# Kernel tuning notes

Hardware: AMD Instinct MI355X
Metric: run time of the kernel (lower is better)

The kernel has to match this reference:

```python
import jax, jax.numpy as jnp
import numpy as np

N_NODES = 50000
N_EDGES = 800000
D = 128  # in_dim == hidden_dim
N_CLASSES = 2


def setup_inputs() -> dict:
    key = jax.random.key(0)
    ks = jax.random.split(key, 8)
    x = jax.random.normal(ks[0], (N_NODES, D), dtype=jnp.float32)
    edge_index = jax.random.randint(ks[1], (2, N_EDGES), 0, N_NODES)
    s = 1.0 / np.sqrt(D)
    W1 = jax.random.normal(ks[2], (D, D), dtype=jnp.float32) * s
    b1 = jnp.zeros((D,), jnp.float32)
    W2 = jax.random.normal(ks[3], (D, D), dtype=jnp.float32) * s
    b2 = jnp.zeros((D,), jnp.float32)
    Wc = jax.random.normal(ks[4], (D, N_CLASSES), dtype=jnp.float32) * s
    bc = jnp.zeros((N_CLASSES,), jnp.float32)
    return {"x": x, "edge_index": edge_index, "W1": W1, "b1": b1,
            "W2": W2, "b2": b2, "Wc": Wc, "bc": bc}


def gcn_layer(x, W, b, src, dst, n):
    """PyG GCNConv: h = D^{-1/2}(A+I)D^{-1/2} (x @ W) + b, self-loops added."""
    h = x @ W  # [n, d_out]
    loop = jnp.arange(n)
    src2 = jnp.concatenate([src, loop])  # [E+n]
    dst2 = jnp.concatenate([dst, loop])
    deg = jax.ops.segment_sum(jnp.ones_like(dst2, dtype=h.dtype), dst2, num_segments=n)
    inv_sqrt = jax.lax.rsqrt(deg)  # deg >= 1 thanks to self-loops
    coef = inv_sqrt[src2] * inv_sqrt[dst2]  # [E+n]
    msg = h[src2] * coef[:, None]  # gather + scale
    out = jax.ops.segment_sum(msg, dst2, num_segments=n)  # scatter-add
    return out + b


def reference(x, edge_index, W1, b1, W2, b2, Wc, bc):
    src, dst = edge_index[0], edge_index[1]
    n = x.shape[0]
    h = jax.nn.relu(gcn_layer(x, W1, b1, src, dst, n))
    h = jax.nn.relu(gcn_layer(h, W2, b2, src, dst, n))
    g = h.mean(axis=0)  # mean pool over nodes -> [hidden]
    logits = g @ Wc + bc  # [2]
    return jax.nn.log_softmax(logits, axis=0)
```

## Files before the change

kernel.cpp:

```cpp
#include <hip/hip_runtime.h>

#define D 128
#define PAD 64
#define SCAP 12288
typedef unsigned char  u8;
typedef unsigned short u16;
typedef unsigned int   u32;
typedef unsigned long long u64;
typedef __attribute__((ext_vector_type(8))) short bf16x8;
typedef __attribute__((ext_vector_type(4))) float f32x4;
typedef __attribute__((ext_vector_type(2))) float f32x2;


__device__ __forceinline__ float b2f_lo(u32 w) {
    u32 x = w << 16; float f; __builtin_memcpy(&f, &x, 4); return f;
}
__device__ __forceinline__ float b2f_hi(u32 w) {
    u32 x = w & 0xffff0000u; float f; __builtin_memcpy(&f, &x, 4); return f;
}
__device__ __forceinline__ u16 f2b(float f) {
    u32 x; __builtin_memcpy(&x, &f, 4);
    u32 lsb = (x >> 16) & 1u;
    x += 0x7fffu + lsb;
    return (u16)(x >> 16);
}
__device__ __forceinline__ u8 f2fp8(float f) {
    int p = __builtin_amdgcn_cvt_pk_fp8_f32(f, f, 0, false);
    return (u8)(p & 0xff);
}
__device__ __forceinline__ f32x2 fp8lo(u32 w) {
    return __builtin_amdgcn_cvt_pk_f32_fp8((int)w, false);
}
__device__ __forceinline__ f32x2 fp8hi(u32 w) {
    return __builtin_amdgcn_cvt_pk_f32_fp8((int)w, true);
}

__global__ void k_init(float* __restrict__ gpool,
                       const void* p0, const void* p1, const void* p2, const void* p3,
                       const void* p4, const void* p5, const void* p6,
                       int* __restrict__ flags, u16* __restrict__ WTf1,
                       u16* __restrict__ WTf2,
                       const int* __restrict__ src, const int* __restrict__ dst, int E,
                       u32* __restrict__ slist, int* __restrict__ slcur, int pb) {
    __shared__ __align__(16) u16 t[128 * 130];
    __shared__ int s_wbf;
    __shared__ u32 lcnt[128], lbase[128], boff[128];
    const int bid = blockIdx.x, tid = threadIdx.x;
    if (bid == 0) {
        uint4* g4 = (uint4*)gpool;
        #pragma unroll
        for (int k = 0; k < 8; ++k) g4[tid + k * 256] = (uint4){0, 0, 0, 0};
        const void* ps[7] = {p0, p1, p2, p3, p4, p5, p6};
        const int   nw[7] = {64, 64, 64, 64, 64, 64, 1};
        int wave = tid >> 6, lane = tid & 63;
        for (int b = wave; b < 7; b += 4) {
            u32 w = (lane < nw[b]) ? ((const u32*)ps[b])[lane] : 0u;
            int nzb = (w != 0u);
            u32 e = (w >> 7) & 0xFFu;
            int hitb = nzb && (e > 100u && e < 140u);
            u64 nzm = __ballot(nzb);
            u64 hm  = __ballot(hitb);
            int nz = __popcll(nzm), hits = __popcll(hm);
            if (lane == 0) flags[b] = (nz == 0) || (2 * hits >= nz);
        }
        return;
    }
    if (bid >= 3) {
        const int pid = bid - 3;
        const int E4 = E >> 2;
        u32* stg = (u32*)t;
        if (tid < 128) lcnt[tid] = 0;
        __syncthreads();
        u32 wpk[8]; int gg[8]; u32 loc[8]; int vld[2];
        #pragma unroll
        for (int h = 0; h < 2; ++h) {
            const int i4 = pid * 512 + h * 256 + tid;
            vld[h] = i4 < E4;
            if (vld[h]) {
                int4 dd = ((const int4*)dst)[i4];
                int4 sv = ((const int4*)src)[i4];
                int d[4] = {dd.x, dd.y, dd.z, dd.w};
                int s[4] = {sv.x, sv.y, sv.z, sv.w};
                #pragma unroll
                for (int k = 0; k < 4; ++k) {
                    int e = h * 4 + k;
                    gg[e]  = d[k] >> 9;
                    wpk[e] = ((u32)d[k] << 16) | (u32)(s[k] & 0xffff);
                    loc[e] = atomicAdd(&lcnt[gg[e]], 1u);
                }
            }
        }
        __syncthreads();
        if (tid < 128) boff[tid] = lcnt[tid];
        __syncthreads();
        for (int o = 1; o < 128; o <<= 1) {
            u32 v = 0;
            if (tid < 128 && tid >= o) v = boff[tid - o];
            __syncthreads();
            if (tid < 128) boff[tid] += v;
            __syncthreads();
        }
        if (tid < 128) {
            u32 c = lcnt[tid];
            lbase[tid] = c ? atomicAdd((u32*)&slcur[tid], c) : 0u;
            boff[tid] -= c;
        }
        __syncthreads();
        #pragma unroll
        for (int h = 0; h < 2; ++h) {
            if (vld[h]) {
                #pragma unroll
                for (int k = 0; k < 4; ++k) {
                    int e = h * 4 + k;
                    stg[boff[gg[e]] + loc[e]] = wpk[e];
                }
            }
        }
        __syncthreads();
        const int tot = (int)(boff[127] + lcnt[127]);
        for (int j = tid; j < tot; j += 256) {
            u32 w = stg[j];
            int g = (int)(w >> 25);
            u32 p = lbase[g] + (u32)j - boff[g];
            if (p < SCAP) slist[(size_t)g * SCAP + p] = w;
        }
        if (pid == pb - 1 && tid < (E & 3)) {
            int e = (E & ~3) + tid;
            int d = dst[e], s = src[e];
            u32 p = atomicAdd((u32*)&slcur[d >> 9], 1u);
            if (p < SCAP) slist[(size_t)(d >> 9) * SCAP + p] = ((u32)d << 16) | (u32)(s & 0xffff);
        }
        return;
    }
    const void* Wp = (bid == 1) ? p1 : p3;
    u16* WTf      = (bid == 1) ? WTf1 : WTf2;
    if (tid < 64) {
        u32 w = ((const u32*)Wp)[tid];
        int nzb = (w != 0u);
        u32 e = (w >> 7) & 0xFFu;
        int hitb = nzb && (e > 100u && e < 140u);
        u64 nzm = __ballot(nzb);
        u64 hm  = __ballot(hitb);
        if (tid == 0) {
            int nz = __popcll(nzm), hits = __popcll(hm);
            s_wbf = (nz == 0) || (2 * hits >= nz);
        }
    }
    __syncthreads();
    if (s_wbf) {
        const u32* W2w = (const u32*)Wp;
        for (int i = tid; i < 8192; i += 256) {
            u32 w = W2w[i];
            int k = i >> 6, n2 = (i & 63) * 2;
            t[k * 130 + n2]     = (u16)(w & 0xffffu);
            t[k * 130 + n2 + 1] = (u16)(w >> 16);
        }
    } else {
        const float* Wf = (const float*)Wp;
        for (int i = tid; i < 16384; i += 256) {
            int k = i >> 7, nn = i & 127;
            t[k * 130 + nn] = f2b(Wf[i]);
        }
    }
    __syncthreads();
    for (int fi = tid; fi < 16384; fi += 256) {
        int j = fi & 7, lane = (fi >> 3) & 63, tc = fi >> 9;
        int tt = tc >> 3, c = tc & 7, m = lane & 15, quad = lane >> 4;
        int k = tt * 32 + quad * 8 + j, col = c * 16 + m;
        WTf[fi] = t[k * 130 + col];
    }
}

__global__ __launch_bounds__(256) void k_fused(
        const void* __restrict__ Ap, const u16* __restrict__ WTf1,
        const int* __restrict__ flags, u8* __restrict__ C, int n, int gb1, int fb0,
        int nsl, const u32* __restrict__ slist, const int* __restrict__ slcur,
        int* __restrict__ cnt, float* __restrict__ inv, u16* __restrict__ csrp) {
    __shared__ __align__(16) u8 sbuf[32768];
    __shared__ int lc[512];
    const int tid = threadIdx.x;
    if (blockIdx.x < (u32)gb1) {
        __shared__ int s_abf;
        u16* wfrag = (u16*)sbuf;
        for (int i = tid; i < 2048; i += 256)
            ((uint4*)wfrag)[i] = ((const uint4*)WTf1)[i];
        if (tid == 0) s_abf = flags[0];
        __syncthreads();
        const int abf = s_abf;
        const int wv = tid >> 6, lane = tid & 63;
        const int m = lane & 15, quad = lane >> 4;
        const int r0 = blockIdx.x * 128 + wv * 32;
        int ar0 = r0 + m;      if (ar0 > n - 1) ar0 = n - 1;
        int ar1 = r0 + 16 + m; if (ar1 > n - 1) ar1 = n - 1;

        bf16x8 a0[4], a1[4];
        if (abf) {
            const u16* A0 = (const u16*)Ap + (size_t)ar0 * D + quad * 8;
            const u16* A1 = (const u16*)Ap + (size_t)ar1 * D + quad * 8;
            #pragma unroll
            for (int t = 0; t < 4; ++t) {
                a0[t] = *(const bf16x8*)(A0 + t * 32);
                a1[t] = *(const bf16x8*)(A1 + t * 32);
            }
        } else {
            const float* A0 = (const float*)Ap + (size_t)ar0 * D + quad * 8;
            const float* A1 = (const float*)Ap + (size_t)ar1 * D + quad * 8;
            #pragma unroll
            for (int t = 0; t < 4; ++t) {
                float4 f0 = *(const float4*)(A0 + t * 32);
                float4 f1 = *(const float4*)(A0 + t * 32 + 4);
                float4 g0 = *(const float4*)(A1 + t * 32);
                float4 g1 = *(const float4*)(A1 + t * 32 + 4);
                bf16x8 a, b;
                a[0] = (short)f2b(f0.x); a[1] = (short)f2b(f0.y);
                a[2] = (short)f2b(f0.z); a[3] = (short)f2b(f0.w);
                a[4] = (short)f2b(f1.x); a[5] = (short)f2b(f1.y);
                a[6] = (short)f2b(f1.z); a[7] = (short)f2b(f1.w);
                b[0] = (short)f2b(g0.x); b[1] = (short)f2b(g0.y);
                b[2] = (short)f2b(g0.z); b[3] = (short)f2b(g0.w);
                b[4] = (short)f2b(g1.x); b[5] = (short)f2b(g1.y);
                b[6] = (short)f2b(g1.z); b[7] = (short)f2b(g1.w);
                a0[t] = a; a1[t] = b;
            }
        }
        f32x4 acc0[8], acc1[8];
        #pragma unroll
        for (int c = 0; c < 8; ++c) {
            acc0[c] = (f32x4){0.f, 0.f, 0.f, 0.f};
            acc1[c] = (f32x4){0.f, 0.f, 0.f, 0.f};
        }
        #pragma unroll
        for (int t = 0; t < 4; ++t) {
            #pragma unroll
            for (int c = 0; c < 8; ++c) {
                bf16x8 b = *(const bf16x8*)(wfrag + ((size_t)(t * 8 + c) * 64 + lane) * 8);
                acc0[c] = __builtin_amdgcn_mfma_f32_16x16x32_bf16(a0[t], b, acc0[c], 0, 0, 0);
                acc1[c] = __builtin_amdgcn_mfma_f32_16x16x32_bf16(a1[t], b, acc1[c], 0, 0, 0);
            }
        }
        __syncthreads();
        #pragma unroll
        for (int c = 0; c < 8; ++c) {
            #pragma unroll
            for (int r = 0; r < 4; ++r) {
                int lr = wv * 32 + quad * 4 + r;
                sbuf[lr * 132 + c * 16 + m]        = f2fp8(acc0[c][r]);
                sbuf[(lr + 16) * 132 + c * 16 + m] = f2fp8(acc1[c][r]);
            }
        }
        __syncthreads();
        int lr = tid >> 1, off = (tid & 1) * 64;
        int grow = blockIdx.x * 128 + lr;
        if (grow < n) {
            const u8* rp = sbuf + lr * 132 + off;
            uint4 v0 = *(const uint4*)(rp);
            uint4 v1 = *(const uint4*)(rp + 16);
            uint4 v2 = *(const uint4*)(rp + 32);
            uint4 v3 = *(const uint4*)(rp + 48);
            u8* gp = C + (size_t)grow * D + off;
            *(uint4*)(gp)      = v0;
            *(uint4*)(gp + 16) = v1;
            *(uint4*)(gp + 32) = v2;
            *(uint4*)(gp + 48) = v3;
        }
        return;
    }
    if (blockIdx.x < (u32)fb0) return;
    const int s = blockIdx.x - fb0;
    if (s >= nsl) return;
    const int base = s << 9;
    lc[tid] = 0; lc[tid + 256] = 0;
    __syncthreads();
    int len = slcur[s]; if (len > SCAP) len = SCAP;
    const u32* sl = slist + (size_t)s * SCAP;
    for (int e = tid; e < len; e += 256) {
        u32 w = sl[e];
        int d = (int)(w >> 16);
        int pos = atomicAdd(&lc[d - base], 1);
        if (pos < PAD) csrp[(size_t)d * PAD + pos] = (u16)(w & 0xffffu);
    }
    __syncthreads();
    #pragma unroll
    for (int i = tid; i < 512; i += 256) {
        int node = base + i;
        if (node < n) {
            int c = lc[i];
            cnt[node] = c;
            inv[node] = rsqrtf(1.0f + (float)c);
        }
    }
}

template<bool PRE>
__device__ __forceinline__ f32x4 agg_row4(int node, int lane, float invd, int mcnt,
                                          const u8* __restrict__ H,
                                          const u16* __restrict__ csrp,
                                          const float* __restrict__ inv,
                                          const void* __restrict__ bias, int bbf) {
    const int q = lane & 31, half = lane >> 5;
    int idx = csrp[(size_t)node * PAD + lane];
    f32x4 acc = (f32x4){0.f, 0.f, 0.f, 0.f};
    const int NP = (mcnt + 1) >> 1;
    int p = 0;
    for (; p + 8 <= NP; p += 8) {
        u32 w[8]; float sc[8]; int ok[8];
        #pragma unroll
        for (int k = 0; k < 8; ++k) {
            int e = 2 * (p + k) + half;
            int s = __shfl(idx, e);
            w[k] = *(const u32*)(H + (size_t)s * D + q * 4);
            if (!PRE) sc[k] = inv[s];
            ok[k] = e < mcnt;
        }
        #pragma unroll
        for (int k = 0; k < 8; ++k) {
            if (ok[k]) {
                f32x2 lo = fp8lo(w[k]), hi = fp8hi(w[k]);
                if (PRE) {
                    acc[0] += lo[0]; acc[1] += lo[1]; acc[2] += hi[0]; acc[3] += hi[1];
                } else {
                    acc[0] = fmaf(lo[0], sc[k], acc[0]);
                    acc[1] = fmaf(lo[1], sc[k], acc[1]);
                    acc[2] = fmaf(hi[0], sc[k], acc[2]);
                    acc[3] = fmaf(hi[1], sc[k], acc[3]);
                }
            }
        }
    }
    for (; p < NP; ++p) {
        int e = 2 * p + half;
        int s = __shfl(idx, e);
        u32 w = *(const u32*)(H + (size_t)s * D + q * 4);
        float sc = PRE ? 1.f : inv[s];
        if (e < mcnt) {
            f32x2 lo = fp8lo(w), hi = fp8hi(w);
            if (PRE) {
                acc[0] += lo[0]; acc[1] += lo[1]; acc[2] += hi[0]; acc[3] += hi[1];
            } else {
                acc[0] = fmaf(lo[0], sc, acc[0]);
                acc[1] = fmaf(lo[1], sc, acc[1]);
                acc[2] = fmaf(hi[0], sc, acc[2]);
                acc[3] = fmaf(hi[1], sc, acc[3]);
            }
        }
    }
    acc[0] += __shfl_xor(acc[0], 32);
    acc[1] += __shfl_xor(acc[1], 32);
    acc[2] += __shfl_xor(acc[2], 32);
    acc[3] += __shfl_xor(acc[3], 32);
    {
        u32 w = *(const u32*)(H + (size_t)node * D + q * 4);
        f32x2 lo = fp8lo(w), hi = fp8hi(w);
        if (PRE) {
            acc[0] += lo[0]; acc[1] += lo[1]; acc[2] += hi[0]; acc[3] += hi[1];
        } else {
            acc[0] = fmaf(lo[0], invd, acc[0]);
            acc[1] = fmaf(lo[1], invd, acc[1]);
            acc[2] = fmaf(hi[0], invd, acc[2]);
            acc[3] = fmaf(hi[1], invd, acc[3]);
        }
    }
    float b0, b1, b2, b3;
    if (bbf) {
        u32 w0 = ((const u32*)bias)[2 * q], w1 = ((const u32*)bias)[2 * q + 1];
        b0 = b2f_lo(w0); b1 = b2f_hi(w0); b2 = b2f_lo(w1); b3 = b2f_hi(w1);
    } else {
        float4 b = ((const float4*)bias)[q];
        b0 = b.x; b1 = b.y; b2 = b.z; b3 = b.w;
    }
    f32x4 o;
    o[0] = fmaxf(fmaf(invd, acc[0], b0), 0.f);
    o[1] = fmaxf(fmaf(invd, acc[1], b1), 0.f);
    o[2] = fmaxf(fmaf(invd, acc[2], b2), 0.f);
    o[3] = fmaxf(fmaf(invd, acc[3], b3), 0.f);
    return o;
}

__global__ __launch_bounds__(256) void k_aggemm(
        const u8* __restrict__ h, const int* __restrict__ cnt,
        const float* __restrict__ inv,
        const u16* __restrict__ csrp, const void* __restrict__ bias,
        const int* __restrict__ flags, int fidx,
        const u16* __restrict__ WTf, u8* __restrict__ C, int n) {
    __shared__ int s_bbf;
    __shared__ __align__(16) float accA[16][132];
    __shared__ float sinv[16];
    if (threadIdx.x == 0) s_bbf = flags[fidx];
    __syncthreads();
    const int wv = threadIdx.x >> 6, lane = threadIdx.x & 63;
    const int base = blockIdx.x * 16;
    #pragma unroll
    for (int i = 0; i < 4; ++i) {
        int m = wv + i * 4;
        int node = base + m;
        f32x4 o = (f32x4){0.f, 0.f, 0.f, 0.f};
        float invd = 0.f;
        if (node < n) {
            int cn = cnt[node];
            invd = rsqrtf(1.0f + (float)cn);
            int mcnt = cn < PAD ? cn : PAD;
            o = agg_row4<false>(node, lane, invd, mcnt, h, csrp, inv, bias, s_bbf);
        }
        if (lane < 32) {
            float4 v = {o[0], o[1], o[2], o[3]};
            *(float4*)&accA[m][4 * lane] = v;
        }
        if (lane == 0) sinv[m] = invd;
    }
    __syncthreads();
    const int m0 = lane & 15, quad = lane >> 4;
    f32x4 acc[2];
    acc[0] = (f32x4){0.f, 0.f, 0.f, 0.f};
    acc[1] = (f32x4){0.f, 0.f, 0.f, 0.f};
    #pragma unroll
    for (int t = 0; t < 4; ++t) {
        const float* ap = &accA[m0][t * 32 + quad * 8];
        float4 f0 = *(const float4*)ap;
        float4 f1 = *(const float4*)(ap + 4);
        bf16x8 a;
        a[0] = (short)f2b(f0.x); a[1] = (short)f2b(f0.y);
        a[2] = (short)f2b(f0.z); a[3] = (short)f2b(f0.w);
        a[4] = (short)f2b(f1.x); a[5] = (short)f2b(f1.y);
        a[6] = (short)f2b(f1.z); a[7] = (short)f2b(f1.w);
        #pragma unroll
        for (int cc = 0; cc < 2; ++cc) {
            int c = wv * 2 + cc;
            bf16x8 b = *(const bf16x8*)(WTf + ((size_t)(t * 8 + c) * 64 + lane) * 8);
            acc[cc] = __builtin_amdgcn_mfma_f32_16x16x32_bf16(a, b, acc[cc], 0, 0, 0);
        }
    }
    #pragma unroll
    for (int cc = 0; cc < 2; ++cc) {
        int c = wv * 2 + cc;
        #pragma unroll
        for (int r = 0; r < 4; ++r) {
            int row = base + quad * 4 + r;
            if (row < n)
                C[(size_t)row * D + c * 16 + m0] = f2fp8(sinv[quad * 4 + r] * acc[cc][r]);
        }
    }
}

__global__ __launch_bounds__(256) void k_agg2p(const u8* __restrict__ h,
                                               const int* __restrict__ cnt,
                                               const u16* __restrict__ csrp,
                                               const void* __restrict__ bias,
                                               const int* __restrict__ flags, int fidx,
                                               float* __restrict__ gpool, int n) {
    __shared__ int s_bbf;
    __shared__ float sacc[4][128];
    if (threadIdx.x == 0) s_bbf = flags[fidx];
    __syncthreads();
    int wv   = threadIdx.x >> 6;
    int lane = threadIdx.x & 63;
    int node = blockIdx.x * 4 + wv;
    f32x4 o = (f32x4){0.f, 0.f, 0.f, 0.f};
    if (node < n) {
        int cn = cnt[node];
        float invd = rsqrtf(1.0f + (float)cn);
        int mcnt = cn < PAD ? cn : PAD;
        o = agg_row4<true>(node, lane, invd, mcnt, h, csrp, nullptr, bias, s_bbf);
    }
    if (lane < 32) {
        float4 v = {o[0], o[1], o[2], o[3]};
        *(float4*)&sacc[wv][4 * lane] = v;
    }
    __syncthreads();
    if (wv == 0) {
        float a = sacc[0][lane] + sacc[1][lane] + sacc[2][lane] + sacc[3][lane];
        float b = sacc[0][lane + 64] + sacc[1][lane + 64] + sacc[2][lane + 64] + sacc[3][lane + 64];
        float* rep = gpool + (size_t)(blockIdx.x & 63) * 128;
        atomicAdd(&rep[lane],      a);
        atomicAdd(&rep[lane + 64], b);
    }
}

__global__ void k_final(const float* __restrict__ gpool, const void* __restrict__ Wc,
                        const void* __restrict__ bc, const int* __restrict__ flags,
                        void* __restrict__ outp, int n) {
    __shared__ float s0[128], s1[128];
    int t = threadIdx.x;
    float acc = 0.f;
    #pragma unroll 8
    for (int r = 0; r < 64; ++r) acc += gpool[r * 128 + t];
    float g = acc / (float)n;
    float w0, w1;
    if (flags[5]) { u32 w = ((const u32*)Wc)[t]; w0 = b2f_lo(w); w1 = b2f_hi(w); }
    else          { float2 w = ((const float2*)Wc)[t]; w0 = w.x; w1 = w.y; }
    s0[t] = g * w0;
    s1[t] = g * w1;
    __syncthreads();
    if (t == 0) {
        float l0, l1;
        if (flags[6]) { u32 b = ((const u32*)bc)[0]; l0 = b2f_lo(b); l1 = b2f_hi(b); }
        else          { const float* b = (const float*)bc; l0 = b[0]; l1 = b[1]; }
        for (int i = 0; i < 128; ++i) { l0 += s0[i]; l1 += s1[i]; }
        float m = fmaxf(l0, l1);
        float lse = m + logf(expf(l0 - m) + expf(l1 - m));
        if (flags[0]) {
            u16* o = (u16*)outp;
            o[0] = f2b(l0 - lse);
            o[1] = f2b(l1 - lse);
        } else {
            float* o = (float*)outp;
            o[0] = l0 - lse;
            o[1] = l1 - lse;
        }
    }
}

extern "C" void kernel_launch(void* const* d_in, const int* in_sizes, int n_in,
                              void* d_out, int out_size, void* d_ws, size_t ws_size,
                              hipStream_t stream) {
    const void* x  = d_in[0];
    const int*  ei = (const int*)d_in[1];
    const void* W1 = d_in[2];
    const void* b1 = d_in[3];
    const void* W2 = d_in[4];
    const void* b2 = d_in[5];
    const void* Wc = d_in[6];
    const void* bc = d_in[7];

    const int n = in_sizes[0] / D;
    const int E = in_sizes[1] / 2;

    char* wsp = (char*)d_ws;
    size_t off = 0;
    auto carve = [&](size_t bytes) -> void* {
        void* p = wsp + off;
        off = (off + bytes + 255) & ~(size_t)255;
        return p;
    };
    const int nsl = (n + 511) >> 9;
    u8*    h0    = (u8*)carve((size_t)n * D);
    u8*    h1    = (u8*)carve((size_t)n * D);
    int*   cnt   = (int*)carve((size_t)n * 4);
    float* inv   = (float*)carve((size_t)n * 4);
    int*   slcur = (int*)carve(128 * 4);
    u16*   csrp  = (u16*)carve((size_t)n * PAD * 2);
    u32*   slist = (u32*)carve((size_t)nsl * SCAP * 4);
    float* gpool = (float*)carve(64 * 128 * 4);
    int*   flags = (int*)carve(16 * 4);
    u16*   WTf1  = (u16*)carve((size_t)D * D * 2);
    u16*   WTf2  = (u16*)carve((size_t)D * D * 2);
    (void)ws_size; (void)n_in; (void)out_size;

    const int* srcI = ei;
    const int* dstI = ei + E;

    const int pb  = ((E >> 2) + 511) / 512;
    const int gb1 = (n + 127) / 128;
    const int fb0 = (gb1 + 7) & ~7;
    const int gb3 = (n + 15) / 16;
    const int ab  = (n + 3) / 4;

    hipMemsetAsync(slcur, 0, 128 * 4, stream);
    k_init  <<<3 + pb, 256, 0, stream>>>(gpool, x, W1, b1, W2, b2, Wc, bc, flags,
                                         WTf1, WTf2, srcI, dstI, E, slist, slcur, pb);
    k_fused <<<fb0 + nsl, 256, 0, stream>>>(x, WTf1, flags, h0, n,
                                            gb1, fb0, nsl, slist, slcur, cnt, inv, csrp);
    k_aggemm<<<gb3, 256, 0, stream>>>(h0, cnt, inv, csrp, b1, flags, 2, WTf2, h1, n);
    k_agg2p <<<ab, 256, 0, stream>>>(h1, cnt, csrp, b2, flags, 4, gpool, n);
    k_final <<<1, 128, 0, stream>>>(gpool, Wc, bc, flags, d_out, n);
}
```

Measured before the change: 179.7 us.

## Regroup edge bucketing with first GEMM and fuse final logits into pooling

Edge bucketing moves out of the init kernel and into the same launch as the first-layer GEMM, so the two independent jobs overlap. The CSR fill becomes its own kernel, launched after bucketing completes. The separate final logits kernel is removed: the last block of the pooling kernel, detected through an atomic counter, computes the classifier and log-softmax. This trades one launch and the serial dependency of bucketing before the GEMM for an extra kernel boundary before the fill and an atomic done-counter per block.

New measurement: 448.5 us. 2.5x slower.

```diff
diff --git a/kernel.cpp b/kernel.cpp
--- a/kernel.cpp
+++ b/kernel.cpp
@@ -35,16 +35,13 @@
     return __builtin_amdgcn_cvt_pk_f32_fp8((int)w, true);
 }
 
-__global__ void k_init(float* __restrict__ gpool,
-                       const void* p0, const void* p1, const void* p2, const void* p3,
-                       const void* p4, const void* p5, const void* p6,
-                       int* __restrict__ flags, u16* __restrict__ WTf1,
-                       u16* __restrict__ WTf2,
-                       const int* __restrict__ src, const int* __restrict__ dst, int E,
-                       u32* __restrict__ slist, int* __restrict__ slcur, int pb) {
+__global__ void k_init3(float* __restrict__ gpool,
+                        const void* p0, const void* p1, const void* p2, const void* p3,
+                        const void* p4, const void* p5, const void* p6,
+                        int* __restrict__ flags, u16* __restrict__ WTf1,
+                        u16* __restrict__ WTf2) {
     __shared__ __align__(16) u16 t[128 * 130];
     __shared__ int s_wbf;
-    __shared__ u32 lcnt[128], lbase[128], boff[128];
     const int bid = blockIdx.x, tid = threadIdx.x;
     if (bid == 0) {
         uint4* g4 = (uint4*)gpool;
@@ -65,73 +62,6 @@
         }
         return;
     }
-    if (bid >= 3) {
-        const int pid = bid - 3;
-        const int E4 = E >> 2;
-        u32* stg = (u32*)t;
-        if (tid < 128) lcnt[tid] = 0;
-        __syncthreads();
-        u32 wpk[8]; int gg[8]; u32 loc[8]; int vld[2];
-        #pragma unroll
-        for (int h = 0; h < 2; ++h) {
-            const int i4 = pid * 512 + h * 256 + tid;
-            vld[h] = i4 < E4;
-            if (vld[h]) {
-                int4 dd = ((const int4*)dst)[i4];
-                int4 sv = ((const int4*)src)[i4];
-                int d[4] = {dd.x, dd.y, dd.z, dd.w};
-                int s[4] = {sv.x, sv.y, sv.z, sv.w};
-                #pragma unroll
-                for (int k = 0; k < 4; ++k) {
-                    int e = h * 4 + k;
-                    gg[e]  = d[k] >> 9;
-                    wpk[e] = ((u32)d[k] << 16) | (u32)(s[k] & 0xffff);
-                    loc[e] = atomicAdd(&lcnt[gg[e]], 1u);
-                }
-            }
-        }
-        __syncthreads();
-        if (tid < 128) boff[tid] = lcnt[tid];
-        __syncthreads();
-        for (int o = 1; o < 128; o <<= 1) {
-            u32 v = 0;
-            if (tid < 128 && tid >= o) v = boff[tid - o];
-            __syncthreads();
-            if (tid < 128) boff[tid] += v;
-            __syncthreads();
-        }
-        if (tid < 128) {
-            u32 c = lcnt[tid];
-            lbase[tid] = c ? atomicAdd((u32*)&slcur[tid], c) : 0u;
-            boff[tid] -= c;
-        }
-        __syncthreads();
-        #pragma unroll
-        for (int h = 0; h < 2; ++h) {
-            if (vld[h]) {
-                #pragma unroll
-                for (int k = 0; k < 4; ++k) {
-                    int e = h * 4 + k;
-                    stg[boff[gg[e]] + loc[e]] = wpk[e];
-                }
-            }
-        }
-        __syncthreads();
-        const int tot = (int)(boff[127] + lcnt[127]);
-        for (int j = tid; j < tot; j += 256) {
-            u32 w = stg[j];
-            int g = (int)(w >> 25);
-            u32 p = lbase[g] + (u32)j - boff[g];
-            if (p < SCAP) slist[(size_t)g * SCAP + p] = w;
-        }
-        if (pid == pb - 1 && tid < (E & 3)) {
-            int e = (E & ~3) + tid;
-            int d = dst[e], s = src[e];
-            u32 p = atomicAdd((u32*)&slcur[d >> 9], 1u);
-            if (p < SCAP) slist[(size_t)(d >> 9) * SCAP + p] = ((u32)d << 16) | (u32)(s & 0xffff);
-        }
-        return;
-    }
     const void* Wp = (bid == 1) ? p1 : p3;
     u16* WTf      = (bid == 1) ? WTf1 : WTf2;
     if (tid < 64) {
@@ -171,16 +101,16 @@
     }
 }
 
-__global__ __launch_bounds__(256) void k_fused(
+__global__ __launch_bounds__(256) void k_mid(
         const void* __restrict__ Ap, const u16* __restrict__ WTf1,
-        const int* __restrict__ flags, u8* __restrict__ C, int n, int gb1, int fb0,
-        int nsl, const u32* __restrict__ slist, const int* __restrict__ slcur,
-        int* __restrict__ cnt, float* __restrict__ inv, u16* __restrict__ csrp) {
+        const int* __restrict__ flags, u8* __restrict__ C, int n, int gb1,
+        const int* __restrict__ src, const int* __restrict__ dst, int E,
+        u32* __restrict__ slist, int* __restrict__ slcur, int pb) {
     __shared__ __align__(16) u8 sbuf[32768];
-    __shared__ int lc[512];
+    __shared__ u32 lcnt[128], lbase[128], boff[128];
+    __shared__ int s_abf;
     const int tid = threadIdx.x;
     if (blockIdx.x < (u32)gb1) {
-        __shared__ int s_abf;
         u16* wfrag = (u16*)sbuf;
         for (int i = tid; i < 2048; i += 256)
             ((uint4*)wfrag)[i] = ((const uint4*)WTf1)[i];
@@ -265,9 +195,79 @@
         }
         return;
     }
-    if (blockIdx.x < (u32)fb0) return;
-    const int s = blockIdx.x - fb0;
-    if (s >= nsl) return;
+    const int pid = blockIdx.x - gb1;
+    const int E4 = E >> 2;
+    u32* stg = (u32*)sbuf;
+    if (tid < 128) lcnt[tid] = 0;
+    __syncthreads();
+    u32 wpk[8]; int gg[8]; u32 loc[8]; int vld[2];
+    #pragma unroll
+    for (int h = 0; h < 2; ++h) {
+        const int i4 = pid * 512 + h * 256 + tid;
+        vld[h] = i4 < E4;
+        if (vld[h]) {
+            int4 dd = ((const int4*)dst)[i4];
+            int4 sv = ((const int4*)src)[i4];
+            int d[4] = {dd.x, dd.y, dd.z, dd.w};
+            int s[4] = {sv.x, sv.y, sv.z, sv.w};
+            #pragma unroll
+            for (int k = 0; k < 4; ++k) {
+                int e = h * 4 + k;
+                gg[e]  = d[k] >> 9;
+                wpk[e] = ((u32)d[k] << 16) | (u32)(s[k] & 0xffff);
+                loc[e] = atomicAdd(&lcnt[gg[e]], 1u);
+            }
+        }
+    }
+    __syncthreads();
+    if (tid < 128) boff[tid] = lcnt[tid];
+    __syncthreads();
+    for (int o = 1; o < 128; o <<= 1) {
+        u32 v = 0;
+        if (tid < 128 && tid >= o) v = boff[tid - o];
+        __syncthreads();
+        if (tid < 128) boff[tid] += v;
+        __syncthreads();
+    }
+    if (tid < 128) {
+        u32 c = lcnt[tid];
+        lbase[tid] = c ? atomicAdd((u32*)&slcur[tid], c) : 0u;
+        boff[tid] -= c;
+    }
+    __syncthreads();
+    #pragma unroll
+    for (int h = 0; h < 2; ++h) {
+        if (vld[h]) {
+            #pragma unroll
+            for (int k = 0; k < 4; ++k) {
+                int e = h * 4 + k;
+                stg[boff[gg[e]] + loc[e]] = wpk[e];
+            }
+        }
+    }
+    __syncthreads();
+    const int tot = (int)(boff[127] + lcnt[127]);
+    for (int j = tid; j < tot; j += 256) {
+        u32 w = stg[j];
+        int g = (int)(w >> 25);
+        u32 p = lbase[g] + (u32)j - boff[g];
+        if (p < SCAP) slist[(size_t)g * SCAP + p] = w;
+    }
+    if (pid == pb - 1 && tid < (E & 3)) {
+        int e = (E & ~3) + tid;
+        int d = dst[e], s = src[e];
+        u32 p = atomicAdd((u32*)&slcur[d >> 9], 1u);
+        if (p < SCAP) slist[(size_t)(d >> 9) * SCAP + p] = ((u32)d << 16) | (u32)(s & 0xffff);
+    }
+}
+
+__global__ __launch_bounds__(256) void k_fill(
+        const u32* __restrict__ slist, const int* __restrict__ slcur,
+        int* __restrict__ cnt, float* __restrict__ inv,
+        u16* __restrict__ csrp, int n) {
+    __shared__ int lc[512];
+    const int tid = threadIdx.x;
+    const int s = blockIdx.x;
     const int base = s << 9;
     lc[tid] = 0; lc[tid + 256] = 0;
     __syncthreads();
@@ -446,10 +446,15 @@
                                                const u16* __restrict__ csrp,
                                                const void* __restrict__ bias,
                                                const int* __restrict__ flags, int fidx,
-                                               float* __restrict__ gpool, int n) {
-    __shared__ int s_bbf;
+                                               float* __restrict__ gpool, int n,
+                                               const void* __restrict__ Wc,
+                                               const void* __restrict__ bc,
+                                               void* __restrict__ outp,
+                                               int* __restrict__ done) {
+    __shared__ int s_bbf, s_last;
     __shared__ float sacc[4][128];
-    if (threadIdx.x == 0) s_bbf = flags[fidx];
+    __shared__ float s0[128], s1[128];
+    if (threadIdx.x == 0) { s_bbf = flags[fidx]; s_last = 0; }
     __syncthreads();
     int wv   = threadIdx.x >> 6;
     int lane = threadIdx.x & 63;
@@ -472,23 +477,28 @@
         float* rep = gpool + (size_t)(blockIdx.x & 63) * 128;
         atomicAdd(&rep[lane],      a);
         atomicAdd(&rep[lane + 64], b);
-    }
-}
-
-__global__ void k_final(const float* __restrict__ gpool, const void* __restrict__ Wc,
-                        const void* __restrict__ bc, const int* __restrict__ flags,
-                        void* __restrict__ outp, int n) {
-    __shared__ float s0[128], s1[128];
-    int t = threadIdx.x;
-    float acc = 0.f;
-    #pragma unroll 8
-    for (int r = 0; r < 64; ++r) acc += gpool[r * 128 + t];
-    float g = acc / (float)n;
-    float w0, w1;
-    if (flags[5]) { u32 w = ((const u32*)Wc)[t]; w0 = b2f_lo(w); w1 = b2f_hi(w); }
-    else          { float2 w = ((const float2*)Wc)[t]; w0 = w.x; w1 = w.y; }
-    s0[t] = g * w0;
-    s1[t] = g * w1;
+        if (lane == 0) {
+            int old = __hip_atomic_fetch_add(done, 1, __ATOMIC_ACQ_REL,
+                                             __HIP_MEMORY_SCOPE_AGENT);
+            s_last = (old == (int)gridDim.x - 1);
+        }
+    }
+    __syncthreads();
+    if (!s_last) return;
+    const int t = threadIdx.x;
+    if (t < 128) {
+        float acc = 0.f;
+        #pragma unroll 8
+        for (int r = 0; r < 64; ++r)
+            acc += __hip_atomic_load(&gpool[r * 128 + t], __ATOMIC_RELAXED,
+                                     __HIP_MEMORY_SCOPE_AGENT);
+        float g = acc / (float)n;
+        float w0, w1;
+        if (flags[5]) { u32 w = ((const u32*)Wc)[t]; w0 = b2f_lo(w); w1 = b2f_hi(w); }
+        else          { float2 w = ((const float2*)Wc)[t]; w0 = w.x; w1 = w.y; }
+        s0[t] = g * w0;
+        s1[t] = g * w1;
+    }
     __syncthreads();
     if (t == 0) {
         float l0, l1;
@@ -498,13 +508,13 @@
         float m = fmaxf(l0, l1);
         float lse = m + logf(expf(l0 - m) + expf(l1 - m));
         if (flags[0]) {
-            u16* o = (u16*)outp;
-            o[0] = f2b(l0 - lse);
-            o[1] = f2b(l1 - lse);
+            u16* o2 = (u16*)outp;
+            o2[0] = f2b(l0 - lse);
+            o2[1] = f2b(l1 - lse);
         } else {
-            float* o = (float*)outp;
-            o[0] = l0 - lse;
-            o[1] = l1 - lse;
+            float* o2 = (float*)outp;
+            o2[0] = l0 - lse;
+            o2[1] = l1 - lse;
         }
     }
 }
@@ -537,6 +547,7 @@
     int*   cnt   = (int*)carve((size_t)n * 4);
     float* inv   = (float*)carve((size_t)n * 4);
     int*   slcur = (int*)carve(128 * 4);
+    int*   done  = (int*)carve(256);
     u16*   csrp  = (u16*)carve((size_t)n * PAD * 2);
     u32*   slist = (u32*)carve((size_t)nsl * SCAP * 4);
     float* gpool = (float*)carve(64 * 128 * 4);
@@ -550,16 +561,16 @@
 
     const int pb  = ((E >> 2) + 511) / 512;
     const int gb1 = (n + 127) / 128;
-    const int fb0 = (gb1 + 7) & ~7;
     const int gb3 = (n + 15) / 16;
     const int ab  = (n + 3) / 4;
 
-    hipMemsetAsync(slcur, 0, 128 * 4, stream);
-    k_init  <<<3 + pb, 256, 0, stream>>>(gpool, x, W1, b1, W2, b2, Wc, bc, flags,
-                                         WTf1, WTf2, srcI, dstI, E, slist, slcur, pb);
-    k_fused <<<fb0 + nsl, 256, 0, stream>>>(x, WTf1, flags, h0, n,
-                                            gb1, fb0, nsl, slist, slcur, cnt, inv, csrp);
+    hipMemsetAsync(slcur, 0, 768, stream);
+    k_init3 <<<3, 256, 0, stream>>>(gpool, x, W1, b1, W2, b2, Wc, bc, flags,
+                                    WTf1, WTf2);
+    k_mid   <<<gb1 + pb, 256, 0, stream>>>(x, WTf1, flags, h0, n, gb1,
+                                           srcI, dstI, E, slist, slcur, pb);
+    k_fill  <<<nsl, 256, 0, stream>>>(slist, slcur, cnt, inv, csrp, n);
     k_aggemm<<<gb3, 256, 0, stream>>>(h0, cnt, inv, csrp, b1, flags, 2, WTf2, h1, n);
-    k_agg2p <<<ab, 256, 0, stream>>>(h1, cnt, csrp, b2, flags, 4, gpool, n);
-    k_final <<<1, 128, 0, stream>>>(gpool, Wc, bc, flags, d_out, n);
-}
+    k_agg2p <<<ab, 256, 0, stream>>>(h1, cnt, csrp, b2, flags, 4, gpool, n,
+                                     Wc, bc, d_out, done);
+}
```
